# Performance work log

Hardware: AMD Instinct MI355X
Metric: run time of the kernel (lower is better)

Reference implementation:

```python
import jax, jax.numpy as jnp
import numpy as np

EXPONENT = 6.0  # lj_exponent
N_NODES = 100_000
N_EDGES = 3_200_000
N_TYPES = 16


def setup_inputs() -> dict:
    key = jax.random.key(0)
    ks = jax.random.split(key, 6)
    sigma = jax.random.uniform(ks[0], (N_TYPES, N_TYPES), dtype=jnp.float32)
    delta = jnp.zeros((N_TYPES, N_TYPES), dtype=jnp.float32)
    epsilon = jax.random.uniform(ks[1], (N_TYPES, N_TYPES), dtype=jnp.float32)
    # realistic interatomic distances in (0.5, 2.5) so r^-6 stays finite
    edge_len = jax.random.uniform(ks[2], (N_EDGES,), dtype=jnp.float32) * 2.0 + 0.5
    edge_cutoff = jax.random.uniform(ks[3], (N_EDGES,), dtype=jnp.float32)
    edge_index = jax.random.randint(ks[4], (2, N_EDGES), 0, N_NODES, dtype=jnp.int64)
    atom_types = jax.random.randint(ks[5], (N_NODES,), 0, N_TYPES, dtype=jnp.int64)
    return {"sigma": sigma, "delta": delta, "epsilon": epsilon,
            "edge_len": edge_len, "edge_cutoff": edge_cutoff,
            "edge_index": edge_index, "atom_types": atom_types}


def _pair_param(param, idx1, idx2):
    # _LJParam: symmetrize the upper-triangular storage, flat-gather per edge, relu
    t = param.shape[0]
    sym = jnp.triu(param) + jnp.triu(param, 1).T        # [T, T]
    return jax.nn.relu(sym.reshape(-1)[idx1 * t + idx2])  # [E]


def reference(sigma, delta, epsilon, edge_len, edge_cutoff, edge_index, atom_types):
    n_nodes = atom_types.shape[0]
    edge_center = edge_index[0]
    # gather per-edge atom types, then per-pair parameters   (lj_style == 'lj')
    idx1 = atom_types[edge_index[0]]  # [E]
    idx2 = atom_types[edge_index[1]]  # [E]
    sig = _pair_param(sigma, idx1, idx2)
    dlt = _pair_param(delta, idx1, idx2)
    eps = _pair_param(epsilon, idx1, idx2)
    x = (sig / (edge_len - dlt)) ** EXPONENT   # (sigma/(r-delta))^p
    lj_eng = 2.0 * eps * (x * x - x)           # 2*eps*((-x) + (-x)^2)
    lj_eng = lj_eng * edge_cutoff              # smooth cutoff envelope
    # scatter-reduce per-edge energies onto center atoms
    atomic_eng = jax.ops.segment_sum(lj_eng, edge_center, num_segments=n_nodes)
    return atomic_eng[:, None]  # [N, 1] per-atom energy ('0e')
```

## Files before the change

### kernel.cpp

```cpp
#include <hip/hip_runtime.h>


#define THREADS  512
#define EPT      8
#define EPB      (THREADS*EPT)
#define STHREADS 256
#define BSHIFT   9
#define BSIZE    512
#define MAXB2    256
#define NMASK    511u
#define LDSWORDS 12544
#define NREP     8

__device__ __forceinline__ float lj_energy(float sig, float dlt, float eps,
                                           float len, float cut) {
    const float r  = sig / (len - dlt);
    const float r2 = r * r;
    const float x  = r2 * r2 * r2;
    return 2.0f * eps * (x * x - x) * cut;
}

__device__ __forceinline__ void load_params(const float* __restrict__ sigma,
                                            const float* __restrict__ delta,
                                            const float* __restrict__ epsilon,
                                            float* s_sig, float* s_dlt, float* s_eps,
                                            int t) {
    if (t < 256) {
        const int i  = t >> 4;
        const int j  = t & 15;
        const int lo = min(i, j);
        const int hi = max(i, j);
        const int src = lo * 16 + hi;
        s_sig[t] = fmaxf(sigma[src],   0.0f);
        s_dlt[t] = fmaxf(delta[src],   0.0f);
        s_eps[t] = fmaxf(epsilon[src], 0.0f);
    }
}

__global__ __launch_bounds__(STHREADS) void pack_types_kernel(
    const int* __restrict__ at, uint32_t* __restrict__ packed,
    uint32_t* __restrict__ gcursor, int n_nodes)
{
    if (blockIdx.x < NREP)
        gcursor[blockIdx.x * 256 + threadIdx.x] = 0u;
    const int w = blockIdx.x * STHREADS + threadIdx.x;
    const int nwords = (n_nodes + 7) >> 3;
    if (w >= nwords) return;
    const int base = w * 8;
    uint32_t v = 0;
    if (base + 8 <= n_nodes) {
        const int4 a = *reinterpret_cast<const int4*>(at + base);
        const int4 b = *reinterpret_cast<const int4*>(at + base + 4);
        v =  (uint32_t)(a.x & 15)        | ((uint32_t)(a.y & 15) << 4)
          | ((uint32_t)(a.z & 15) << 8)  | ((uint32_t)(a.w & 15) << 12)
          | ((uint32_t)(b.x & 15) << 16) | ((uint32_t)(b.y & 15) << 20)
          | ((uint32_t)(b.z & 15) << 24) | ((uint32_t)(b.w & 15) << 28);
    } else {
        for (int k = 0; k < 8; ++k) {
            const int idx = base + k;
            const uint32_t tv = (idx < n_nodes) ? (uint32_t)(at[idx] & 15) : 0u;
            v |= tv << (4 * k);
        }
    }
    packed[w] = v;
}

__global__ __launch_bounds__(THREADS) void lj_fused(
    const float* __restrict__ sigma,
    const float* __restrict__ delta,
    const float* __restrict__ epsilon,
    const float* __restrict__ edge_len,
    const float* __restrict__ edge_cutoff,
    const int*  __restrict__ edge_index,
    const uint32_t* __restrict__ packedT,
    uint32_t* __restrict__ gcursor,
    uint32_t* __restrict__ pairs,
    int n_edges, int n_nodes, int nbucket, int REGr)
{
    __shared__ float s_sig[256], s_dlt[256], s_eps[256];
    __shared__ __align__(16) uint32_t typeT[LDSWORDS];
    __shared__ uint32_t hist[MAXB2];
    __shared__ uint32_t lbase[MAXB2];
    __shared__ uint32_t gbase[MAXB2];
    __shared__ uint32_t stage[EPB];

    const int t = threadIdx.x;
    load_params(sigma, delta, epsilon, s_sig, s_dlt, s_eps, t);
    if (t < MAXB2) hist[t] = 0u;

    const int nwords = (n_nodes + 7) >> 3;
    {
        const int nw4 = nwords >> 2;
        const uint4* s4 = reinterpret_cast<const uint4*>(packedT);
        uint4* d4 = reinterpret_cast<uint4*>(typeT);
        for (int i = t; i < nw4; i += THREADS) d4[i] = s4[i];
        for (int i = (nw4 << 2) + t; i < nwords; i += THREADS) typeT[i] = packedT[i];
    }
    __syncthreads();

    #define TYPE_OF(idx) ((typeT[(idx) >> 3] >> (((idx) & 7) << 2)) & 15u)

    const int blk     = blockIdx.x;
    const int rep8    = blk & (NREP - 1);
    const int blkbase = blk * EPB;
    const int nval    = min(EPB, n_edges - blkbase);

    uint32_t pk[EPT];
    int      bk[EPT];
    #pragma unroll
    for (int i = 0; i < EPT / 4; ++i) {
        const int g = blkbase + i * (THREADS * 4) + t * 4;
        if (g + 3 < n_edges) {
            const int4   ctr = *reinterpret_cast<const int4*>(edge_index + g);
            const int4   oth = *reinterpret_cast<const int4*>(edge_index + n_edges + g);
            const float4 len = *reinterpret_cast<const float4*>(edge_len + g);
            const float4 cut = *reinterpret_cast<const float4*>(edge_cutoff + g);
            const int   c[4] = {ctr.x, ctr.y, ctr.z, ctr.w};
            const int   o[4] = {oth.x, oth.y, oth.z, oth.w};
            const float L[4] = {len.x, len.y, len.z, len.w};
            const float C[4] = {cut.x, cut.y, cut.z, cut.w};
            #pragma unroll
            for (int k = 0; k < 4; ++k) {
                const int fl = (int)((TYPE_OF(c[k]) << 4) | TYPE_OF(o[k]));
                const float e = lj_energy(s_sig[fl], s_dlt[fl], s_eps[fl], L[k], C[k]);
                pk[i*4+k] = (__float_as_uint(e) & ~NMASK) | (uint32_t)(c[k] & NMASK);
                bk[i*4+k] = c[k] >> BSHIFT;
                atomicAdd(&hist[bk[i*4+k]], 1u);
            }
        } else {
            #pragma unroll
            for (int k = 0; k < 4; ++k) {
                const int e_idx = g + k;
                if (e_idx < n_edges) {
                    const int ci = edge_index[e_idx];
                    const int oi = edge_index[n_edges + e_idx];
                    const int fl = (int)((TYPE_OF(ci) << 4) | TYPE_OF(oi));
                    const float e = lj_energy(s_sig[fl], s_dlt[fl], s_eps[fl],
                                              edge_len[e_idx], edge_cutoff[e_idx]);
                    pk[i*4+k] = (__float_as_uint(e) & ~NMASK) | (uint32_t)(ci & NMASK);
                    bk[i*4+k] = ci >> BSHIFT;
                    atomicAdd(&hist[bk[i*4+k]], 1u);
                } else {
                    bk[i*4+k] = -1;
                }
            }
        }
    }
    __syncthreads();

    if (t < 64) {
        uint32_t v[4]; uint32_t s = 0;
        #pragma unroll
        for (int k = 0; k < 4; ++k) {
            const uint32_t tmp = hist[t * 4 + k];
            v[k] = s; s += tmp;
        }
        uint32_t inc = s;
        #pragma unroll
        for (int off = 1; off < 64; off <<= 1) {
            const uint32_t u = __shfl_up(inc, off, 64);
            if (t >= off) inc += u;
        }
        const uint32_t lane_excl = inc - s;
        #pragma unroll
        for (int k = 0; k < 4; ++k) {
            const uint32_t e = lane_excl + v[k];
            lbase[t * 4 + k] = e;
            hist[t * 4 + k]  = e;
        }
    }
    __syncthreads();

    if (t < MAXB2 / 2) {
        const int b0 = 2 * t, b1 = 2 * t + 1;
        const uint32_t l0 = lbase[b0];
        const uint32_t l1 = lbase[b1];
        const uint32_t l2 = (b1 + 1 < MAXB2) ? lbase[b1 + 1] : (uint32_t)nval;
        const uint32_t cnt0 = l1 - l0;
        const uint32_t cnt1 = l2 - l1;
        if ((cnt0 | cnt1) != 0u) {
            unsigned long long* g64 =
                reinterpret_cast<unsigned long long*>(gcursor + rep8 * 256) + t;
            const unsigned long long add =
                (unsigned long long)cnt0 | ((unsigned long long)cnt1 << 32);
            const unsigned long long old = atomicAdd(g64, add);
            gbase[b0] = (uint32_t)old;
            gbase[b1] = (uint32_t)(old >> 32);
        }
    }
    #pragma unroll
    for (int j = 0; j < EPT; ++j) {
        if (bk[j] >= 0) {
            const uint32_t r = atomicAdd(&hist[bk[j]], 1u);
            stage[r] = pk[j];
        }
    }
    __syncthreads();

    const int grp = t >> 3;
    const int lig = t & 7;
    for (int b = grp; b < nbucket; b += 64) {
        const uint32_t l0 = lbase[b];
        const uint32_t l1 = (b + 1 < MAXB2) ? lbase[b + 1] : (uint32_t)nval;
        const uint32_t cnt = l1 - l0;
        const uint32_t base = gbase[b];
        const uint32_t avail = (base < (uint32_t)REGr)
                             ? min(cnt, (uint32_t)REGr - base) : 0u;
        uint32_t* dst = pairs + ((size_t)b * NREP + rep8) * REGr + base;
        for (uint32_t j = lig; j < avail; j += 8)
            dst[j] = stage[l0 + j];
    }
}

__global__ __launch_bounds__(THREADS) void lj_accum_direct(
    const uint32_t* __restrict__ pairs,
    const uint32_t* __restrict__ gcursor,
    float* __restrict__ out,
    int REGr, int n_nodes)
{
    __shared__ float acc[4][BSIZE];
    const int t = threadIdx.x;
    const int b = blockIdx.x;

    #pragma unroll
    for (int w = 0; w < 4; ++w) acc[w][t] = 0.0f;
    __syncthreads();

    const int wave = t >> 6;
    const int lane = t & 63;
    const uint32_t cnt = min(gcursor[wave * 256 + b], (uint32_t)REGr);
    const uint32_t* seg = pairs + ((size_t)b * NREP + wave) * REGr;
    const int ar = wave & 3;
    for (uint32_t i = lane; i < cnt; i += 64) {
        const uint32_t p = seg[i];
        atomicAdd(&acc[ar][p & NMASK], __uint_as_float(p & ~NMASK));
    }
    __syncthreads();

    const long long n = (long long)b * BSIZE + t;
    if (n < n_nodes)
        out[n] = acc[0][t] + acc[1][t] + acc[2][t] + acc[3][t];
}

__global__ __launch_bounds__(STHREADS) void lj_scatter_direct(
    const float* __restrict__ sigma,
    const float* __restrict__ delta,
    const float* __restrict__ epsilon,
    const float* __restrict__ edge_len,
    const float* __restrict__ edge_cutoff,
    const int*  __restrict__ edge_index,
    const int*  __restrict__ atom_types,
    float* __restrict__ out,
    int n_edges)
{
    __shared__ float s_sig[256], s_dlt[256], s_eps[256];
    const int t = threadIdx.x;
    load_params(sigma, delta, epsilon, s_sig, s_dlt, s_eps, t);
    __syncthreads();

    const int base = (blockIdx.x * STHREADS + t) * 4;
    if (base >= n_edges) return;
    const int lim = min(base + 4, n_edges);
    for (int e = base; e < lim; ++e) {
        const int ci = edge_index[e];
        const int oi = edge_index[n_edges + e];
        const int fl = (atom_types[ci] << 4) | atom_types[oi];
        const float en = lj_energy(s_sig[fl], s_dlt[fl], s_eps[fl],
                                   edge_len[e], edge_cutoff[e]);
        atomicAdd(out + ci, en);
    }
}

static inline size_t align16(size_t x) { return (x + 15) & ~(size_t)15; }

extern "C" void kernel_launch(void* const* d_in, const int* in_sizes, int n_in,
                              void* d_out, int out_size, void* d_ws, size_t ws_size,
                              hipStream_t stream) {
    const float* sigma       = (const float*)d_in[0];
    const float* delta       = (const float*)d_in[1];
    const float* epsilon     = (const float*)d_in[2];
    const float* edge_len    = (const float*)d_in[3];
    const float* edge_cutoff = (const float*)d_in[4];
    const int*   edge_index  = (const int*)d_in[5];
    const int*   atom_types  = (const int*)d_in[6];
    float*       out         = (float*)d_out;

    const int n_edges = in_sizes[3];
    const int n_nodes = in_sizes[6];

    const int nblk    = (n_edges + EPB - 1) / EPB;
    const int nbucket = (n_nodes + BSIZE - 1) / BSIZE;
    const int nwords  = (n_nodes + 7) >> 3;

    int REGr = 2 * (n_edges / (nbucket > 0 ? nbucket * NREP : NREP));
    REGr = ((REGr + 511) / 512) * 512;
    if (REGr < 1024) REGr = 1024;

    const size_t gcur_bytes   = align16((size_t)NREP * 256 * sizeof(uint32_t));
    const size_t packed_bytes = align16((size_t)nwords * sizeof(uint32_t));
    const size_t pairs_bytes  = align16((size_t)nbucket * NREP * REGr * sizeof(uint32_t));
    const size_t need = gcur_bytes + packed_bytes + pairs_bytes;

    if (nbucket <= MAXB2 && nwords <= LDSWORDS && ws_size >= need) {
        char* p = (char*)d_ws;
        uint32_t* gcursor = (uint32_t*)p;  p += gcur_bytes;
        uint32_t* packed  = (uint32_t*)p;  p += packed_bytes;
        uint32_t* pairs   = (uint32_t*)p;

        const int pgrid = max((nwords + STHREADS - 1) / STHREADS, NREP);
        pack_types_kernel<<<pgrid, STHREADS, 0, stream>>>(
            atom_types, packed, gcursor, n_nodes);

        lj_fused<<<nblk, THREADS, 0, stream>>>(
            sigma, delta, epsilon, edge_len, edge_cutoff,
            edge_index, packed, gcursor, pairs, n_edges, n_nodes, nbucket, REGr);

        lj_accum_direct<<<nbucket, THREADS, 0, stream>>>(
            pairs, gcursor, out, REGr, n_nodes);
    } else {
        hipMemsetAsync(d_out, 0, (size_t)out_size * sizeof(float), stream);
        const int grid = (n_edges + STHREADS * 4 - 1) / (STHREADS * 4);
        lj_scatter_direct<<<grid, STHREADS, 0, stream>>>(
            sigma, delta, epsilon, edge_len, edge_cutoff,
            edge_index, atom_types, out, n_edges);
    }
}
```

Before: 54.36 us.

## Overlap global bucket reservation with scan and flatten staged copy-out

The global atomic reservation of bucket slots now runs from the raw histogram in separate waves, at the same time as the local prefix scan. This removes one block-wide barrier and takes the global atomics off the scan's critical path. The copy-out changes from per-bucket groups of 8 lanes to a flat loop over staged entries. Each entry's bucket id is kept in a byte array, which balances work across threads at the cost of extra LDS traffic. The accumulate kernel also gets one LDS accumulator row per wave (8 instead of 4) to cut atomic contention, at the cost of more shared memory.

```diff
diff --git a/kernel.cpp b/kernel.cpp
--- a/kernel.cpp
+++ b/kernel.cpp
@@ -80,9 +80,11 @@
     __shared__ float s_sig[256], s_dlt[256], s_eps[256];
     __shared__ __align__(16) uint32_t typeT[LDSWORDS];
     __shared__ uint32_t hist[MAXB2];
+    __shared__ uint32_t cursor[MAXB2];
     __shared__ uint32_t lbase[MAXB2];
     __shared__ uint32_t gbase[MAXB2];
     __shared__ uint32_t stage[EPB];
+    __shared__ unsigned char stageb[EPB];
 
     const int t = threadIdx.x;
     load_params(sigma, delta, epsilon, s_sig, s_dlt, s_eps, t);
@@ -148,6 +150,21 @@
     }
     __syncthreads();
 
+    if (t >= 64 && t < 192) {
+        const int p  = t - 64;
+        const int b0 = 2 * p, b1 = 2 * p + 1;
+        const uint32_t cnt0 = hist[b0];
+        const uint32_t cnt1 = hist[b1];
+        if ((cnt0 | cnt1) != 0u) {
+            unsigned long long* g64 =
+                reinterpret_cast<unsigned long long*>(gcursor + rep8 * 256) + p;
+            const unsigned long long add =
+                (unsigned long long)cnt0 | ((unsigned long long)cnt1 << 32);
+            const unsigned long long old = atomicAdd(g64, add);
+            gbase[b0] = (uint32_t)old;
+            gbase[b1] = (uint32_t)(old >> 32);
+        }
+    }
     if (t < 64) {
         uint32_t v[4]; uint32_t s = 0;
         #pragma unroll
@@ -165,50 +182,27 @@
         #pragma unroll
         for (int k = 0; k < 4; ++k) {
             const uint32_t e = lane_excl + v[k];
-            lbase[t * 4 + k] = e;
-            hist[t * 4 + k]  = e;
-        }
-    }
-    __syncthreads();
-
-    if (t < MAXB2 / 2) {
-        const int b0 = 2 * t, b1 = 2 * t + 1;
-        const uint32_t l0 = lbase[b0];
-        const uint32_t l1 = lbase[b1];
-        const uint32_t l2 = (b1 + 1 < MAXB2) ? lbase[b1 + 1] : (uint32_t)nval;
-        const uint32_t cnt0 = l1 - l0;
-        const uint32_t cnt1 = l2 - l1;
-        if ((cnt0 | cnt1) != 0u) {
-            unsigned long long* g64 =
-                reinterpret_cast<unsigned long long*>(gcursor + rep8 * 256) + t;
-            const unsigned long long add =
-                (unsigned long long)cnt0 | ((unsigned long long)cnt1 << 32);
-            const unsigned long long old = atomicAdd(g64, add);
-            gbase[b0] = (uint32_t)old;
-            gbase[b1] = (uint32_t)(old >> 32);
-        }
-    }
+            lbase[t * 4 + k]  = e;
+            cursor[t * 4 + k] = e;
+        }
+    }
+    __syncthreads();
+
     #pragma unroll
     for (int j = 0; j < EPT; ++j) {
         if (bk[j] >= 0) {
-            const uint32_t r = atomicAdd(&hist[bk[j]], 1u);
-            stage[r] = pk[j];
-        }
-    }
-    __syncthreads();
-
-    const int grp = t >> 3;
-    const int lig = t & 7;
-    for (int b = grp; b < nbucket; b += 64) {
-        const uint32_t l0 = lbase[b];
-        const uint32_t l1 = (b + 1 < MAXB2) ? lbase[b + 1] : (uint32_t)nval;
-        const uint32_t cnt = l1 - l0;
-        const uint32_t base = gbase[b];
-        const uint32_t avail = (base < (uint32_t)REGr)
-                             ? min(cnt, (uint32_t)REGr - base) : 0u;
-        uint32_t* dst = pairs + ((size_t)b * NREP + rep8) * REGr + base;
-        for (uint32_t j = lig; j < avail; j += 8)
-            dst[j] = stage[l0 + j];
+            const uint32_t r = atomicAdd(&cursor[bk[j]], 1u);
+            stage[r]  = pk[j];
+            stageb[r] = (unsigned char)bk[j];
+        }
+    }
+    __syncthreads();
+
+    for (int i = t; i < nval; i += THREADS) {
+        const int b = (int)stageb[i];
+        const uint32_t pos = gbase[b] + ((uint32_t)i - lbase[b]);
+        if (pos < (uint32_t)REGr)
+            pairs[((size_t)b * NREP + rep8) * REGr + pos] = stage[i];
     }
 }
 
@@ -218,28 +212,31 @@
     float* __restrict__ out,
     int REGr, int n_nodes)
 {
-    __shared__ float acc[4][BSIZE];
+    __shared__ float acc[NREP][BSIZE];
     const int t = threadIdx.x;
     const int b = blockIdx.x;
 
     #pragma unroll
-    for (int w = 0; w < 4; ++w) acc[w][t] = 0.0f;
+    for (int w = 0; w < NREP; ++w) acc[w][t] = 0.0f;
     __syncthreads();
 
     const int wave = t >> 6;
     const int lane = t & 63;
     const uint32_t cnt = min(gcursor[wave * 256 + b], (uint32_t)REGr);
     const uint32_t* seg = pairs + ((size_t)b * NREP + wave) * REGr;
-    const int ar = wave & 3;
     for (uint32_t i = lane; i < cnt; i += 64) {
         const uint32_t p = seg[i];
-        atomicAdd(&acc[ar][p & NMASK], __uint_as_float(p & ~NMASK));
+        atomicAdd(&acc[wave][p & NMASK], __uint_as_float(p & ~NMASK));
     }
     __syncthreads();
 
     const long long n = (long long)b * BSIZE + t;
-    if (n < n_nodes)
-        out[n] = acc[0][t] + acc[1][t] + acc[2][t] + acc[3][t];
+    if (n < n_nodes) {
+        float s = 0.0f;
+        #pragma unroll
+        for (int w = 0; w < NREP; ++w) s += acc[w][t];
+        out[n] = s;
+    }
 }
 
 __global__ __launch_bounds__(STHREADS) void lj_scatter_direct(
```

Result: no change. 53.52 us (median of 2 runs) (-1.5%).
